# Kernel optimization log

Measured on AMD Instinct MI355X. Metric: run time of the kernel, lower is better.

The kernel has to match this reference:

```python
import jax, jax.numpy as jnp
import numpy as np

B, N, P, E, H, D, F, L = 16, 500, 100, 128, 8, 16, 512, 6
CLIP = 10.0  # logit_clipping


def _heads(x, h):
    b, n, _ = x.shape
    return x.reshape(b, n, h, -1).transpose(0, 2, 1, 3)  # [b,h,n,d]


def _mha(q, k, v, mask3=None):
    d = q.shape[-1]
    s = jnp.einsum('bhnd,bhmd->bhnm', q, k) / jnp.sqrt(jnp.asarray(d, q.dtype))
    if mask3 is not None:
        s = s + mask3[:, None, :, :]
    w = jax.nn.softmax(s, axis=-1)
    o = jnp.einsum('bhnm,bhmd->bhnd', w, v)
    b, h, n, dd = o.shape
    return o.transpose(0, 2, 1, 3).reshape(b, n, h * dd)


def _ff(x, w1, b1, w2, b2):
    return jax.nn.relu(x @ w1 + b1) @ w2 + b2


def _forward(depot_xy, node_xy, node_demand, load, cur_dist, ninf_mask,
             emb_depot_w, emb_depot_b, emb_node_w, emb_node_b,
             enc_wq, enc_wk, enc_wv, enc_comb_w, enc_comb_b,
             enc_ff1_w, enc_ff1_b, enc_ff2_w, enc_ff2_b,
             dec_wq_last, dec_wk, dec_wv, dec_comb_w, dec_comb_b,
             dec_cap_w, dec_ff1_w, dec_ff1_b, dec_ff2_w, dec_ff2_b,
             current_node):
    # ---------------- encoder ----------------
    node_xy_demand = jnp.concatenate([node_xy, node_demand[:, :, None]], axis=2)  # [B,N,3]
    x = jnp.concatenate([depot_xy @ emb_depot_w + emb_depot_b,
                         node_xy_demand @ emb_node_w + emb_node_b], axis=1)  # [B,N+1,E]
    for i in range(L):
        q = _heads(x @ enc_wq[i], H)
        k = _heads(x @ enc_wk[i], H)
        v = _heads(x @ enc_wv[i], H)
        mh = _mha(q, k, v) @ enc_comb_w[i] + enc_comb_b[i]
        o1 = x + mh
        x = o1 + _ff(o1, enc_ff1_w[i], enc_ff1_b[i], enc_ff2_w[i], enc_ff2_b[i])
    encoded_nodes = x  # [B, N+1, E]
    # decoder kv cache (set_kv)
    k = _heads(encoded_nodes @ dec_wk, H)
    v = _heads(encoded_nodes @ dec_wv, H)
    # ---------------- one decode step ----------------
    encoded_last = jnp.take_along_axis(encoded_nodes, current_node[:, :, None], axis=1)  # [B,P,E]
    input_cat = jnp.concatenate([encoded_last, load[:, :, None]], axis=2)  # [B,P,E+1]
    q = _heads(input_cat @ dec_wq_last, H)
    mh = _mha(q, k, v, mask3=ninf_mask) @ dec_comb_w + dec_comb_b
    mh = mh + encoded_last + load[:, :, None] @ dec_cap_w
    q_ref = _ff(mh, dec_ff1_w, dec_ff1_b, dec_ff2_w, dec_ff2_b) + mh
    score = jnp.einsum('bpe,bne->bpn', q_ref, encoded_nodes) / jnp.sqrt(jnp.asarray(E, q_ref.dtype))
    # distance-based noise injection
    dmin = cur_dist.min(axis=-1, keepdims=True)
    dmax = cur_dist.max(axis=-1, keepdims=True)
    norm_dist = (cur_dist - dmin) / (dmax - dmin + 1e-6)
    problem_size = ninf_mask.shape[2]
    nm = 50.0 / problem_size
    base_noise = jax.random.normal(jax.random.key(42), cur_dist.shape, cur_dist.dtype) * 0.2 + 0.5
    score = score - (1.0 - nm) * jnp.log(norm_dist + 1e-6) + base_noise * nm
    score = CLIP * jnp.tanh(score) + ninf_mask
    return jax.nn.softmax(score, axis=2)  # [B,P,N+1]


def setup_inputs() -> dict:
    key = jax.random.key(0)
    ks = iter(jax.random.split(key, 40))
    def rn(shape, s=0.02):
        return s * jax.random.normal(next(ks), shape, jnp.float32)
    return dict(
        depot_xy=jax.random.uniform(next(ks), (B, 1, 2), jnp.float32),
        node_xy=jax.random.uniform(next(ks), (B, N, 2), jnp.float32),
        node_demand=jax.random.uniform(next(ks), (B, N), jnp.float32),
        load=jax.random.uniform(next(ks), (B, P), jnp.float32),
        cur_dist=jax.random.uniform(next(ks), (B, P, N + 1), jnp.float32),
        ninf_mask=jnp.zeros((B, P, N + 1), jnp.float32),
        current_node=jax.random.randint(next(ks), (B, P), 0, N + 1),
        emb_depot_w=rn((2, E)), emb_depot_b=rn((E,)),
        emb_node_w=rn((3, E)), emb_node_b=rn((E,)),
        enc_wq=rn((L, E, H * D)), enc_wk=rn((L, E, H * D)), enc_wv=rn((L, E, H * D)),
        enc_comb_w=rn((L, H * D, E)), enc_comb_b=rn((L, E)),
        enc_ff1_w=rn((L, E, F)), enc_ff1_b=rn((L, F)),
        enc_ff2_w=rn((L, F, E)), enc_ff2_b=rn((L, E)),
        dec_wq_last=rn((E + 1, H * D)), dec_wk=rn((E, H * D)), dec_wv=rn((E, H * D)),
        dec_comb_w=rn((H * D, E)), dec_comb_b=rn((E,)),
        dec_cap_w=rn((1, E)),
        dec_ff1_w=rn((E, F)), dec_ff1_b=rn((F,)),
        dec_ff2_w=rn((F, E)), dec_ff2_b=rn((E,)),
    )


def reference(depot_xy, node_xy, node_demand, load, cur_dist, ninf_mask, current_node,
              emb_depot_w, emb_depot_b, emb_node_w, emb_node_b,
              enc_wq, enc_wk, enc_wv, enc_comb_w, enc_comb_b,
              enc_ff1_w, enc_ff1_b, enc_ff2_w, enc_ff2_b,
              dec_wq_last, dec_wk, dec_wv, dec_comb_w, dec_comb_b,
              dec_cap_w, dec_ff1_w, dec_ff1_b, dec_ff2_w, dec_ff2_b):
    return _forward(depot_xy, node_xy, node_demand, load, cur_dist, ninf_mask,
                    emb_depot_w, emb_depot_b, emb_node_w, emb_node_b,
                    enc_wq, enc_wk, enc_wv, enc_comb_w, enc_comb_b,
                    enc_ff1_w, enc_ff1_b, enc_ff2_w, enc_ff2_b,
                    dec_wq_last, dec_wk, dec_wv, dec_comb_w, dec_comb_b,
                    dec_cap_w, dec_ff1_w, dec_ff1_b, dec_ff2_w, dec_ff2_b,
                    current_node)
```

## Files before the change

kernel.cpp:

```cpp
#include <hip/hip_runtime.h>
#include <math.h>

#define Bb 16
#define Nn 500
#define NT 501
#define Pp 100
#define Ee 128
#define Hh 8
#define Dd 16
#define Ff 512
#define Ll 6
#define Mtok (Bb*NT)
#define PR (Bb*Pp)
#define TJ 32
#define SPLIT 4
#define KSEG 126
#define DSPLIT 16
#define DSEG 32
#define ENCP (6*128*384)
#define DECP (128*256)
#define SNP 512
#define KP 36

typedef __attribute__((ext_vector_type(8))) short bf16x8;
typedef __attribute__((ext_vector_type(4))) float f32x4;

__device__ __forceinline__ unsigned short bfhi(float x){
  union { float f; unsigned u; } c; c.f = x; return (unsigned short)(c.u >> 16);
}
__device__ __forceinline__ float bff(unsigned short h){
  union { float f; unsigned u; } c; c.u = ((unsigned)h) << 16; return c.f;
}
__device__ __forceinline__ uint2 pack4(unsigned short a, unsigned short b,
                                       unsigned short c, unsigned short d){
  uint2 r; r.x = (unsigned)a | ((unsigned)b << 16);
  r.y = (unsigned)c | ((unsigned)d << 16); return r;
}

__global__ __launch_bounds__(256) void pack_k(
    const float* __restrict__ ewq, const float* __restrict__ ewk, const float* __restrict__ ewv,
    const float* __restrict__ dwk, const float* __restrict__ dwv,
    float* __restrict__ encP, float* __restrict__ decP)
{
  int i = blockIdx.x*256 + threadIdx.x;
  if (i < ENCP) {
    int l = i / (128*384); int rem = i - l*128*384; int k = rem / 384; int n = rem - k*384;
    float v;
    if (n < 128)      v = ewq[((size_t)l*128 + k)*128 + n];
    else if (n < 256) v = ewk[((size_t)l*128 + k)*128 + (n-128)];
    else              v = ewv[((size_t)l*128 + k)*128 + (n-256)];
    encP[i] = v;
  } else {
    int j = i - ENCP;
    if (j < DECP) {
      int k = j >> 8; int n = j & 255;
      decP[j] = (n < 128) ? dwk[k*128 + n] : dwv[k*128 + (n-128)];
    }
  }
}

__global__ __launch_bounds__(256) void embed_k(
    const float* __restrict__ depot_xy, const float* __restrict__ node_xy,
    const float* __restrict__ node_demand,
    const float* __restrict__ wD, const float* __restrict__ bD,
    const float* __restrict__ wN, const float* __restrict__ bN,
    float* __restrict__ x)
{
  int t = blockIdx.x*256 + threadIdx.x;
  if (t >= Mtok*Ee) return;
  int e   = t & (Ee-1);
  int tok = t >> 7;
  int b   = tok / NT;
  int n   = tok - b*NT;
  float v;
  if (n == 0) {
    v = depot_xy[b*2+0]*wD[0*Ee+e] + depot_xy[b*2+1]*wD[1*Ee+e] + bD[e];
  } else {
    int nn = n - 1;
    float c0 = node_xy[(b*Nn + nn)*2 + 0];
    float c1 = node_xy[(b*Nn + nn)*2 + 1];
    float c2 = node_demand[b*Nn + nn];
    v = c0*wN[0*Ee+e] + c1*wN[1*Ee+e] + c2*wN[2*Ee+e] + bN[e];
  }
  x[(size_t)tok*Ee + e] = v;
}

__global__ __launch_bounds__(256) void gemm_k(
    const float* __restrict__ A, const float* __restrict__ W,
    const float* __restrict__ bias, const float* __restrict__ res,
    float* __restrict__ C, int M, int N, int K, int relu)
{
  __shared__ __align__(16) unsigned short Ah[2][64][KP];
  __shared__ __align__(16) unsigned short Al[2][64][KP];
  __shared__ __align__(16) unsigned short Bh[2][64][KP];
  __shared__ __align__(16) unsigned short Bl[2][64][KP];

  int tid = threadIdx.x;
  int m0 = blockIdx.x * 64, n0 = blockIdx.y * 64;
  int wvid = tid >> 6;
  int lane = tid & 63;
  int lrow = lane & 15;
  int lk8  = (lane >> 4) * 8;

  f32x4 acc0 = {0.f,0.f,0.f,0.f}, acc1 = acc0, acc2 = acc0, acc3 = acc0;

  int ar = tid >> 2;
  int ac = (tid & 3) << 2;
  int wr = tid >> 4;
  int wc = (tid & 15) << 2;

  const float* Ap = A + (size_t)(m0 + ar)*K + ac;
  const float* Wp = W + (size_t)wr*N + n0 + wc;
  bool aok = (m0 + ar) < M;

  float4 zz = make_float4(0.f,0.f,0.f,0.f);
  float4 av0 = aok ? *(const float4*)(Ap)      : zz;
  float4 av1 = aok ? *(const float4*)(Ap + 16) : zz;
  float4 wv0 = *(const float4*)(Wp);
  float4 wv1 = *(const float4*)(Wp + (size_t)16*N);

  int nk = K >> 5;
  for (int t = 0; t < nk; ++t) {
    int cur = t & 1;
    {
      unsigned short h0=bfhi(av0.x), h1=bfhi(av0.y), h2=bfhi(av0.z), h3=bfhi(av0.w);
      unsigned short l0=bfhi(av0.x-bff(h0)), l1=bfhi(av0.y-bff(h1)),
                     l2=bfhi(av0.z-bff(h2)), l3=bfhi(av0.w-bff(h3));
      *(uint2*)&Ah[cur][ar][ac] = pack4(h0,h1,h2,h3);
      *(uint2*)&Al[cur][ar][ac] = pack4(l0,l1,l2,l3);
      h0=bfhi(av1.x); h1=bfhi(av1.y); h2=bfhi(av1.z); h3=bfhi(av1.w);
      l0=bfhi(av1.x-bff(h0)); l1=bfhi(av1.y-bff(h1));
      l2=bfhi(av1.z-bff(h2)); l3=bfhi(av1.w-bff(h3));
      *(uint2*)&Ah[cur][ar][ac+16] = pack4(h0,h1,h2,h3);
      *(uint2*)&Al[cur][ar][ac+16] = pack4(l0,l1,l2,l3);
    }
    {
      float w4[4] = {wv0.x, wv0.y, wv0.z, wv0.w};
      #pragma unroll
      for (int i=0;i<4;i++){
        unsigned short h = bfhi(w4[i]);
        Bh[cur][wc+i][wr] = h;
        Bl[cur][wc+i][wr] = bfhi(w4[i] - bff(h));
      }
      float w5[4] = {wv1.x, wv1.y, wv1.z, wv1.w};
      #pragma unroll
      for (int i=0;i<4;i++){
        unsigned short h = bfhi(w5[i]);
        Bh[cur][wc+i][wr+16] = h;
        Bl[cur][wc+i][wr+16] = bfhi(w5[i] - bff(h));
      }
    }
    __syncthreads();
    if (t+1 < nk) {
      av0 = aok ? *(const float4*)(Ap + (size_t)(t+1)*32)      : zz;
      av1 = aok ? *(const float4*)(Ap + (size_t)(t+1)*32 + 16) : zz;
      wv0 = *(const float4*)(Wp + (size_t)(t+1)*32*N);
      wv1 = *(const float4*)(Wp + ((size_t)(t+1)*32 + 16)*N);
    }
    union FR { bf16x8 v; uint2 u[2]; };
    FR ah, al;
    ah.u[0] = *(const uint2*)&Ah[cur][wvid*16 + lrow][lk8];
    ah.u[1] = *(const uint2*)&Ah[cur][wvid*16 + lrow][lk8+4];
    al.u[0] = *(const uint2*)&Al[cur][wvid*16 + lrow][lk8];
    al.u[1] = *(const uint2*)&Al[cur][wvid*16 + lrow][lk8+4];
    #define DOFRAG(f, accv) { \
      FR bh, bl; \
      bh.u[0] = *(const uint2*)&Bh[cur][(f)*16 + lrow][lk8]; \
      bh.u[1] = *(const uint2*)&Bh[cur][(f)*16 + lrow][lk8+4]; \
      bl.u[0] = *(const uint2*)&Bl[cur][(f)*16 + lrow][lk8]; \
      bl.u[1] = *(const uint2*)&Bl[cur][(f)*16 + lrow][lk8+4]; \
      accv = __builtin_amdgcn_mfma_f32_16x16x32_bf16(ah.v, bh.v, accv, 0,0,0); \
      accv = __builtin_amdgcn_mfma_f32_16x16x32_bf16(ah.v, bl.v, accv, 0,0,0); \
      accv = __builtin_amdgcn_mfma_f32_16x16x32_bf16(al.v, bh.v, accv, 0,0,0); \
    }
    DOFRAG(0, acc0); DOFRAG(1, acc1); DOFRAG(2, acc2); DOFRAG(3, acc3);
    #undef DOFRAG
  }

  int crow0 = m0 + wvid*16 + (lane >> 4)*4;
  int col0  = n0 + lrow;
  #define WRFRAG(f, accv) { \
    int col = col0 + (f)*16; \
    float bvs = bias ? bias[col] : 0.f; \
    _Pragma("unroll") \
    for (int j=0;j<4;j++){ \
      int row = crow0 + j; \
      if (row < M) { \
        float v = accv[j] + bvs; \
        if (relu) v = fmaxf(v, 0.f); \
        if (res) v += res[(size_t)row*N + col]; \
        C[(size_t)row*N + col] = v; \
      } \
    } \
  }
  WRFRAG(0, acc0); WRFRAG(1, acc1); WRFRAG(2, acc2); WRFRAG(3, acc3);
  #undef WRFRAG
}

__device__ __forceinline__ float dot4(float4 a, float4 b){
  return fmaf(a.x,b.x, fmaf(a.y,b.y, fmaf(a.z,b.z, a.w*b.w)));
}

__global__ __launch_bounds__(256, 1) void attn_enc_k(
    const float* __restrict__ QKV, float* __restrict__ part_o,
    float* __restrict__ part_l)
{
  int blk = blockIdx.x;
  int s  = blk % SPLIT;
  int bh = blk / SPLIT;
  int h  = bh & (Hh-1);
  int b  = bh >> 3;
  int tid = threadIdx.x;
  int p0 = tid;
  int p1 = tid + 256;
  const int klo = s*KSEG;
  int kseg = NT - klo; if (kseg > KSEG) kseg = KSEG;

  __shared__ __align__(16) float4 Ks[2][TJ][4];
  __shared__ __align__(16) float4 Vs[2][TJ][4];

  int row = (tid >> 2) & 31;
  int lc  = tid & 3;
  bool isV = tid >= 128;
  const int kvoff = isV ? 256 : 128;

  bool vbq = p1 < NT;

  const float4* qp0 = (const float4*)(QKV + ((size_t)(b*NT + p0))*384 + h*Dd);
  float4 qa0=qp0[0], qa1=qp0[1], qa2=qp0[2], qa3=qp0[3];
  float4 qb0,qb1,qb2,qb3;
  if (vbq) {
    const float4* qp1 = (const float4*)(QKV + ((size_t)(b*NT + p1))*384 + h*Dd);
    qb0=qp1[0]; qb1=qp1[1]; qb2=qp1[2]; qb3=qp1[3];
  } else {
    qb0=qb1=qb2=qb3=make_float4(0,0,0,0);
  }

  if (row < kseg) {
    float4 v = *((const float4*)(QKV + ((size_t)(b*NT + klo + row))*384 + kvoff + h*Dd) + lc);
    if (isV) Vs[0][row][lc] = v; else Ks[0][row][lc] = v;
  }
  __syncthreads();

  float lA = 0.f, lB = 0.f;
  float4 oA0=make_float4(0,0,0,0), oA1=oA0, oA2=oA0, oA3=oA0;
  float4 oB0=oA0, oB1=oA0, oB2=oA0, oB3=oA0;
  const int ntiles = (kseg + TJ - 1)/TJ;
  int buf = 0;

  for (int t = 0; t < ntiles; ++t) {
    int j0 = t*TJ;
    if (t+1 < ntiles) {
      int jj = j0 + TJ + row;
      if (jj < kseg) {
        float4 v = *((const float4*)(QKV + ((size_t)(b*NT + klo + jj))*384 + kvoff + h*Dd) + lc);
        if (isV) Vs[buf^1][row][lc] = v; else Ks[buf^1][row][lc] = v;
      }
    }
    int jend = kseg - j0; if (jend > TJ) jend = TJ;

    #pragma unroll 2
    for (int jj = 0; jj < jend; ++jj) {
      float4 k0=Ks[buf][jj][0], k1=Ks[buf][jj][1], k2=Ks[buf][jj][2], k3=Ks[buf][jj][3];
      float sA = (dot4(qa0,k0)+dot4(qa1,k1)) + (dot4(qa2,k2)+dot4(qa3,k3));
      float sB = (dot4(qb0,k0)+dot4(qb1,k1)) + (dot4(qb2,k2)+dot4(qb3,k3));
      float wA = __expf(sA*0.25f);
      float wB = __expf(sB*0.25f);
      lA += wA; lB += wB;
      float4 v0=Vs[buf][jj][0], v1=Vs[buf][jj][1], v2=Vs[buf][jj][2], v3=Vs[buf][jj][3];
      oA0.x=fmaf(wA,v0.x,oA0.x); oA0.y=fmaf(wA,v0.y,oA0.y); oA0.z=fmaf(wA,v0.z,oA0.z); oA0.w=fmaf(wA,v0.w,oA0.w);
      oA1.x=fmaf(wA,v1.x,oA1.x); oA1.y=fmaf(wA,v1.y,oA1.y); oA1.z=fmaf(wA,v1.z,oA1.z); oA1.w=fmaf(wA,v1.w,oA1.w);
      oA2.x=fmaf(wA,v2.x,oA2.x); oA2.y=fmaf(wA,v2.y,oA2.y); oA2.z=fmaf(wA,v2.z,oA2.z); oA2.w=fmaf(wA,v2.w,oA2.w);
      oA3.x=fmaf(wA,v3.x,oA3.x); oA3.y=fmaf(wA,v3.y,oA3.y); oA3.z=fmaf(wA,v3.z,oA3.z); oA3.w=fmaf(wA,v3.w,oA3.w);
      oB0.x=fmaf(wB,v0.x,oB0.x); oB0.y=fmaf(wB,v0.y,oB0.y); oB0.z=fmaf(wB,v0.z,oB0.z); oB0.w=fmaf(wB,v0.w,oB0.w);
      oB1.x=fmaf(wB,v1.x,oB1.x); oB1.y=fmaf(wB,v1.y,oB1.y); oB1.z=fmaf(wB,v1.z,oB1.z); oB1.w=fmaf(wB,v1.w,oB1.w);
      oB2.x=fmaf(wB,v2.x,oB2.x); oB2.y=fmaf(wB,v2.y,oB2.y); oB2.z=fmaf(wB,v2.z,oB2.z); oB2.w=fmaf(wB,v2.w,oB2.w);
      oB3.x=fmaf(wB,v3.x,oB3.x); oB3.y=fmaf(wB,v3.y,oB3.y); oB3.z=fmaf(wB,v3.z,oB3.z); oB3.w=fmaf(wB,v3.w,oB3.w);
    }
    __syncthreads();
    buf ^= 1;
  }

  size_t r0 = ((size_t)s*128 + bh)*NT + p0;
  float4* po0 = (float4*)(part_o + r0*16);
  po0[0]=oA0; po0[1]=oA1; po0[2]=oA2; po0[3]=oA3;
  part_l[r0] = lA;
  if (vbq) {
    size_t r1 = ((size_t)s*128 + bh)*NT + p1;
    float4* po1 = (float4*)(part_o + r1*16);
    po1[0]=oB0; po1[1]=oB1; po1[2]=oB2; po1[3]=oB3;
    part_l[r1] = lB;
  }
}

__global__ __launch_bounds__(256) void comb_gemm_k(
    const float* __restrict__ part_o, const float* __restrict__ part_l,
    const float* __restrict__ W, const float* __restrict__ bias,
    const float* __restrict__ res, float* __restrict__ C)
{
  __shared__ __align__(16) float As[2][16][68];
  __shared__ __align__(16) float Bs[2][16][68];
  int tid = threadIdx.x;
  int tx = tid & 15, ty = tid >> 4;
  int m0 = blockIdx.x * 64, n0 = blockIdx.y * 64;
  float acc[4][4];
  #pragma unroll
  for (int i=0;i<4;i++)
    #pragma unroll
    for (int j=0;j<4;j++) acc[i][j] = 0.f;

  int ar = tid >> 2;
  int ak = (tid & 3) << 2;
  int br = tid >> 4;
  int bc = (tid & 15) << 2;

  int row = m0 + ar;
  bool aok = row < Mtok;
  int tok = aok ? row : 0;
  int bb = tok / NT;
  int p  = tok - bb*NT;
  const size_t pbase = ((size_t)(bb*8))*NT + p;

  const float* Wp = W + (size_t)br*Ee + n0 + bc;

  #define LOADA(t, dst) { \
    float4 o4 = make_float4(0.f,0.f,0.f,0.f); float l = 0.f; \
    _Pragma("unroll") \
    for (int s=0;s<SPLIT;s++){ \
      size_t idx = (size_t)s*((size_t)128*NT) + pbase + (size_t)(t)*NT; \
      float4 v = *(const float4*)(part_o + idx*16 + ak); \
      o4.x+=v.x; o4.y+=v.y; o4.z+=v.z; o4.w+=v.w; \
      l += part_l[idx]; \
    } \
    float inv = aok ? 1.f/l : 0.f; \
    dst = make_float4(o4.x*inv, o4.y*inv, o4.z*inv, o4.w*inv); \
  }

  float4 av; LOADA(0, av);
  float4 wv = *(const float4*)(Wp);

  for (int t = 0; t < 8; ++t) {
    int cur = t & 1;
    As[cur][ak+0][ar] = av.x; As[cur][ak+1][ar] = av.y;
    As[cur][ak+2][ar] = av.z; As[cur][ak+3][ar] = av.w;
    *(float4*)(&Bs[cur][br][bc]) = wv;
    __syncthreads();
    if (t+1 < 8) {
      LOADA(t+1, av);
      wv = *(const float4*)(Wp + (size_t)(t+1)*16*Ee);
    }
    #pragma unroll
    for (int k=0;k<16;k++){
      float4 a4 = *(const float4*)(&As[cur][k][ty*4]);
      float4 b4 = *(const float4*)(&Bs[cur][k][tx*4]);
      float avv[4] = {a4.x,a4.y,a4.z,a4.w};
      float bvv[4] = {b4.x,b4.y,b4.z,b4.w};
      #pragma unroll
      for (int i=0;i<4;i++)
        #pragma unroll
        for (int j=0;j<4;j++)
          acc[i][j] = fmaf(avv[i], bvv[j], acc[i][j]);
    }
  }
  #undef LOADA

  float4 bv = *(const float4*)(bias + n0 + tx*4);
  #pragma unroll
  for (int i=0;i<4;i++){
    int orow = m0 + ty*4 + i;
    if (orow >= Mtok) continue;
    float4 o;
    float4 rv = *(const float4*)(res + (size_t)orow*Ee + n0 + tx*4);
    o.x = acc[i][0] + bv.x + rv.x; o.y = acc[i][1] + bv.y + rv.y;
    o.z = acc[i][2] + bv.z + rv.z; o.w = acc[i][3] + bv.w + rv.w;
    *(float4*)(C + (size_t)orow*Ee + n0 + tx*4) = o;
  }
}

__global__ __launch_bounds__(128) void attn_dec_k(
    const float* __restrict__ Q, const float* __restrict__ KV,
    const float* __restrict__ mask,
    float* __restrict__ part_o, float* __restrict__ part_l)
{
  int blk = blockIdx.x;
  int s  = blk & (DSPLIT-1);
  int bh = blk >> 4;
  int h  = bh & (Hh-1);
  int b  = bh >> 3;
  int klo = s*DSEG;
  int kn  = NT - klo; if (kn > DSEG) kn = DSEG;

  __shared__ __align__(16) float4 Ks[DSEG][4];
  __shared__ __align__(16) float4 Vs[DSEG][4];

  int tid = threadIdx.x;
  for (int i = tid; i < kn*8; i += 128) {
    int row  = i >> 3;
    int q8   = i & 7;
    int quad = q8 & 3;
    int isv  = q8 >> 2;
    float4 v = *(const float4*)(KV + ((size_t)(b*NT + klo + row))*256 + isv*128 + h*Dd + quad*4);
    if (isv) Vs[row][quad] = v; else Ks[row][quad] = v;
  }
  __syncthreads();

  int p = tid;
  if (p >= Pp) return;
  int r = b*Pp + p;
  const float4* qp = (const float4*)(Q + (size_t)r*Ee + h*Dd);
  float4 qa=qp[0], qb=qp[1], qc=qp[2], qd=qp[3];
  const float* mrow = mask + (size_t)r*NT + klo;

  float l = 0.f;
  float4 o0=make_float4(0,0,0,0), o1=o0, o2=o0, o3=o0;
  for (int j=0;j<kn;++j){
    float sc = (dot4(qa,Ks[j][0])+dot4(qb,Ks[j][1])) + (dot4(qc,Ks[j][2])+dot4(qd,Ks[j][3]));
    float w = __expf(sc*0.25f + mrow[j]);
    l += w;
    float4 v0=Vs[j][0],v1=Vs[j][1],v2=Vs[j][2],v3=Vs[j][3];
    o0.x=fmaf(w,v0.x,o0.x); o0.y=fmaf(w,v0.y,o0.y); o0.z=fmaf(w,v0.z,o0.z); o0.w=fmaf(w,v0.w,o0.w);
    o1.x=fmaf(w,v1.x,o1.x); o1.y=fmaf(w,v1.y,o1.y); o1.z=fmaf(w,v1.z,o1.z); o1.w=fmaf(w,v1.w,o1.w);
    o2.x=fmaf(w,v2.x,o2.x); o2.y=fmaf(w,v2.y,o2.y); o2.z=fmaf(w,v2.z,o2.z); o2.w=fmaf(w,v2.w,o2.w);
    o3.x=fmaf(w,v3.x,o3.x); o3.y=fmaf(w,v3.y,o3.y); o3.z=fmaf(w,v3.z,o3.z); o3.w=fmaf(w,v3.w,o3.w);
  }

  size_t rb = ((size_t)s*PR + r)*Hh + h;
  float4* po = (float4*)(part_o + rb*16);
  po[0]=o0; po[1]=o1; po[2]=o2; po[3]=o3;
  part_l[rb] = l;
}

__global__ __launch_bounds__(128) void decq_k(
    const float* __restrict__ x, const int* __restrict__ cur,
    const float* __restrict__ loadv, const float* __restrict__ Wq,
    float* __restrict__ q, float* __restrict__ encl)
{
  __shared__ float row[Ee];
  int r = blockIdx.x, e = threadIdx.x;
  int b = r / Pp;
  int node = cur[r];
  float xv = x[((size_t)(b*NT + node))*Ee + e];
  encl[(size_t)r*Ee + e] = xv;
  row[e] = xv;
  __syncthreads();
  float acc = 0.f;
  #pragma unroll 4
  for (int k=0;k<Ee;k++) acc = fmaf(row[k], Wq[k*128 + e], acc);
  acc = fmaf(loadv[r], Wq[Ee*128 + e], acc);
  q[(size_t)r*128 + e] = acc;
}

__global__ __launch_bounds__(128) void dec_comb_k(
    const float* __restrict__ dpart_o, const float* __restrict__ dpart_l,
    const float* __restrict__ W, const float* __restrict__ bias,
    const float* __restrict__ encl, const float* __restrict__ loadv,
    const float* __restrict__ capw, float* __restrict__ mh)
{
  __shared__ float row[Ee];
  int r = blockIdx.x, e = threadIdx.x;
  int h = e >> 4, d = e & 15;
  const size_t S = (size_t)PR*Hh;
  size_t rb = (size_t)r*Hh + h;
  float L = 0.f, o = 0.f;
  #pragma unroll
  for (int s=0;s<DSPLIT;s++){
    L += dpart_l[(size_t)s*S + rb];
    o += dpart_o[((size_t)s*S + rb)*16 + d];
  }
  row[e] = o / L;
  __syncthreads();
  float acc = 0.f;
  #pragma unroll 4
  for (int k=0;k<Ee;k++) acc = fmaf(row[k], W[k*Ee + e], acc);
  mh[(size_t)r*Ee + e] = acc + bias[e] + encl[(size_t)r*Ee + e] + loadv[r]*capw[e];
}

__global__ __launch_bounds__(256) void xt_k(
    const float* __restrict__ x, float* __restrict__ xT)
{
  __shared__ float T[32][33];
  int n0 = blockIdx.x * 32;
  int k0 = blockIdx.y * 32;
  int b  = blockIdx.z;
  int t  = threadIdx.x;
  int row = t >> 3;
  int c4  = (t & 7) << 2;

  int n = n0 + row;
  float4 v = make_float4(0.f,0.f,0.f,0.f);
  if (n < NT) v = *(const float4*)(x + ((size_t)(b*NT + n))*Ee + k0 + c4);
  T[c4+0][row] = v.x; T[c4+1][row] = v.y; T[c4+2][row] = v.z; T[c4+3][row] = v.w;
  __syncthreads();

  const float SC = 0.08838834764831845f;
  float4 o;
  o.x = T[row][c4+0]*SC; o.y = T[row][c4+1]*SC;
  o.z = T[row][c4+2]*SC; o.w = T[row][c4+3]*SC;
  *(float4*)(xT + ((size_t)(b*Ee + k0 + row))*SNP + n0 + c4) = o;
}

__global__ __launch_bounds__(256) void score_gemm_k(
    const float* __restrict__ qref, const float* __restrict__ xT,
    float* __restrict__ score)
{
  __shared__ __align__(16) float As[2][16][68];
  __shared__ __align__(16) float Bs[2][16][68];
  int tid = threadIdx.x;
  int tx = tid & 15, ty = tid >> 4;
  int m0 = blockIdx.x * 64;
  int n0 = blockIdx.y * 64;
  int b  = blockIdx.z;

  const float* A = qref + (size_t)b*Pp*Ee;
  const float* W = xT   + (size_t)b*Ee*SNP;
  float*       C = score + (size_t)b*Pp*SNP;

  float acc[4][4];
  #pragma unroll
  for (int i=0;i<4;i++)
    #pragma unroll
    for (int j=0;j<4;j++) acc[i][j] = 0.f;

  int ar = tid >> 2;
  int ak = (tid & 3) << 2;
  int br = tid >> 4;
  int bc = (tid & 15) << 2;

  const float* Ap = A + (size_t)(m0 + ar)*Ee + ak;
  const float* Wp = W + (size_t)br*SNP + n0 + bc;
  bool aok = (m0 + ar) < Pp;

  float4 av = aok ? *(const float4*)(Ap) : make_float4(0.f,0.f,0.f,0.f);
  float4 wv = *(const float4*)(Wp);

  for (int t = 0; t < 8; ++t) {
    int cur = t & 1;
    As[cur][ak+0][ar] = av.x; As[cur][ak+1][ar] = av.y;
    As[cur][ak+2][ar] = av.z; As[cur][ak+3][ar] = av.w;
    *(float4*)(&Bs[cur][br][bc]) = wv;
    __syncthreads();
    if (t+1 < 8) {
      av = aok ? *(const float4*)(Ap + (t+1)*16) : make_float4(0.f,0.f,0.f,0.f);
      wv = *(const float4*)(Wp + (size_t)(t+1)*16*SNP);
    }
    #pragma unroll
    for (int k=0;k<16;k++){
      float4 a4 = *(const float4*)(&As[cur][k][ty*4]);
      float4 b4 = *(const float4*)(&Bs[cur][k][tx*4]);
      float avv[4] = {a4.x,a4.y,a4.z,a4.w};
      float bvv[4] = {b4.x,b4.y,b4.z,b4.w};
      #pragma unroll
      for (int i=0;i<4;i++)
        #pragma unroll
        for (int j=0;j<4;j++)
          acc[i][j] = fmaf(avv[i], bvv[j], acc[i][j]);
    }
    __syncthreads();
  }

  #pragma unroll
  for (int i=0;i<4;i++){
    int row = m0 + ty*4 + i;
    if (row >= Pp) continue;
    float4 o;
    o.x = acc[i][0]; o.y = acc[i][1]; o.z = acc[i][2]; o.w = acc[i][3];
    *(float4*)(C + (size_t)row*SNP + n0 + tx*4) = o;
  }
}

__device__ __forceinline__ unsigned rotl32(unsigned x, int r){ return (x<<r)|(x>>(32-r)); }

__device__ float tf_normal(unsigned idx)
{
  unsigned x0 = 0u;
  unsigned x1 = idx;
  const unsigned ks[3] = {0u, 42u, 0u ^ 42u ^ 0x1BD11BDAu};
  x0 += ks[0]; x1 += ks[1];
  const int rotA[4] = {13,15,26,6};
  const int rotB[4] = {17,29,16,24};
  #pragma unroll
  for (int i=0;i<5;i++){
    #pragma unroll
    for (int q=0;q<4;q++){
      int rr = (i&1) ? rotB[q] : rotA[q];
      x0 += x1; x1 = rotl32(x1, rr); x1 ^= x0;
    }
    x0 += ks[(i+1)%3];
    x1 += ks[(i+2)%3] + (unsigned)(i+1);
  }
  unsigned bits = x0 ^ x1;
  float f = __uint_as_float((bits >> 9) | 0x3f800000u) - 1.0f;
  const float lo = -0.99999994f;
  float u = f * 2.0f + lo;
  u = fmaxf(lo, u);
  float w = -log1pf(-u*u);
  float p;
  if (w < 5.0f) {
    w -= 2.5f;
    p = 2.81022636e-08f;
    p = fmaf(p, w, 3.43273939e-07f);
    p = fmaf(p, w, -3.5233877e-06f);
    p = fmaf(p, w, -4.39150654e-06f);
    p = fmaf(p, w, 0.00021858087f);
    p = fmaf(p, w, -0.00125372503f);
    p = fmaf(p, w, -0.00417768164f);
    p = fmaf(p, w, 0.246640727f);
    p = fmaf(p, w, 1.50140941f);
  } else {
    w = sqrtf(w) - 3.0f;
    p = -0.000200214257f;
    p = fmaf(p, w, 0.000100950558f);
    p = fmaf(p, w, 0.00134934322f);
    p = fmaf(p, w, -0.00367342844f);
    p = fmaf(p, w, 0.00573950773f);
    p = fmaf(p, w, -0.0076224613f);
    p = fmaf(p, w, 0.00943887047f);
    p = fmaf(p, w, 1.00167406f);
    p = fmaf(p, w, 2.83297682f);
  }
  return 1.4142135623730951f * (p * u);
}

__global__ __launch_bounds__(512) void final_k(
    const float* __restrict__ score, const float* __restrict__ cur_dist,
    const float* __restrict__ ninf, float* __restrict__ out)
{
  __shared__ float smn[8], smx[8], sm2[8], ss[8];
  const float NM = (float)(50.0/501.0);
  const float C1 = (float)(1.0 - 50.0/501.0);
  int r = blockIdx.x;
  int t = threadIdx.x;
  int wid = t >> 6, lane = t & 63;

  float cd = 0.f;
  float mn = 1e30f, mx = -1e30f;
  if (t < NT) { cd = cur_dist[(size_t)r*NT + t]; mn = cd; mx = cd; }
  #pragma unroll
  for (int off=32; off>=1; off>>=1){
    mn = fminf(mn, __shfl_xor(mn, off));
    mx = fmaxf(mx, __shfl_xor(mx, off));
  }
  if (lane == 0){ smn[wid] = mn; smx[wid] = mx; }
  __syncthreads();
  float dmin = smn[0], dmax = smx[0];
  #pragma unroll
  for (int i=1;i<8;i++){ dmin = fminf(dmin, smn[i]); dmax = fmaxf(dmax, smx[i]); }

  float sval = -1e30f;
  if (t < NT) {
    float nd = (cd - dmin) / (dmax - dmin + 1e-6f);
    float z  = tf_normal((unsigned)r*501u + (unsigned)t);
    float s  = score[(size_t)r*SNP + t] - C1*logf(nd + 1e-6f) + (z*0.2f + 0.5f)*NM;
    sval = 10.0f*tanhf(s) + ninf[(size_t)r*NT + t];
  }
  float mv = sval;
  #pragma unroll
  for (int off=32; off>=1; off>>=1) mv = fmaxf(mv, __shfl_xor(mv, off));
  if (lane == 0) sm2[wid] = mv;
  __syncthreads();
  float smax = sm2[0];
  #pragma unroll
  for (int i=1;i<8;i++) smax = fmaxf(smax, sm2[i]);

  float e = (t < NT) ? expf(sval - smax) : 0.f;
  float sv = e;
  #pragma unroll
  for (int off=32; off>=1; off>>=1) sv += __shfl_xor(sv, off);
  if (lane == 0) ss[wid] = sv;
  __syncthreads();
  float ssum = ss[0];
  #pragma unroll
  for (int i=1;i<8;i++) ssum += ss[i];

  if (t < NT) out[(size_t)r*NT + t] = e / ssum;
}

extern "C" void kernel_launch(void* const* d_in, const int* in_sizes, int n_in,
                              void* d_out, int out_size, void* d_ws, size_t ws_size,
                              hipStream_t stream)
{
  (void)in_sizes; (void)n_in; (void)out_size; (void)ws_size;
  const float* depot_xy    = (const float*)d_in[0];
  const float* node_xy     = (const float*)d_in[1];
  const float* node_demand = (const float*)d_in[2];
  const float* loadv       = (const float*)d_in[3];
  const float* cur_dist    = (const float*)d_in[4];
  const float* ninf        = (const float*)d_in[5];
  const int*   cur_node    = (const int*)d_in[6];
  const float* emb_depot_w = (const float*)d_in[7];
  const float* emb_depot_b = (const float*)d_in[8];
  const float* emb_node_w  = (const float*)d_in[9];
  const float* emb_node_b  = (const float*)d_in[10];
  const float* enc_wq      = (const float*)d_in[11];
  const float* enc_wk      = (const float*)d_in[12];
  const float* enc_wv      = (const float*)d_in[13];
  const float* enc_comb_w  = (const float*)d_in[14];
  const float* enc_comb_b  = (const float*)d_in[15];
  const float* enc_ff1_w   = (const float*)d_in[16];
  const float* enc_ff1_b   = (const float*)d_in[17];
  const float* enc_ff2_w   = (const float*)d_in[18];
  const float* enc_ff2_b   = (const float*)d_in[19];
  const float* dec_wq_last = (const float*)d_in[20];
  const float* dec_wk      = (const float*)d_in[21];
  const float* dec_wv      = (const float*)d_in[22];
  const float* dec_comb_w  = (const float*)d_in[23];
  const float* dec_comb_b  = (const float*)d_in[24];
  const float* dec_cap_w   = (const float*)d_in[25];
  const float* dec_ff1_w   = (const float*)d_in[26];
  const float* dec_ff1_b   = (const float*)d_in[27];
  const float* dec_ff2_w   = (const float*)d_in[28];
  const float* dec_ff2_b   = (const float*)d_in[29];

  float* ws = (float*)d_ws;
  const size_t SZ = (size_t)Mtok*Ee;
  float* xb    = ws + 0*SZ;
  float* qkvb  = ws + 1*SZ;
  float* atb   = ws + 4*SZ;
  float* o1b   = ws + 5*SZ;
  float* ffb   = ws + 6*SZ;
  float* encPk = ws + 10*SZ;
  float* decPk = encPk + ENCP;
  float* part_o  = ffb;
  float* epart_l = atb;
  float* dpart_o = ffb;
  float* dpart_l = o1b;
  float* encl  = qkvb + 2*SZ;
  float* qdec  = encl + 204800;
  float* mhb   = qdec + 204800;
  float* qrefb = atb;
  float* ffh2  = ffb;
  float* xTb   = ffb;
  float* scoreb= o1b;

  pack_k<<<(ENCP + DECP + 255)/256, 256, 0, stream>>>(
      enc_wq, enc_wk, enc_wv, dec_wk, dec_wv, encPk, decPk);

  embed_k<<<(Mtok*Ee + 255)/256, 256, 0, stream>>>(
      depot_xy, node_xy, node_demand, emb_depot_w, emb_depot_b,
      emb_node_w, emb_node_b, xb);

  dim3 gqkv((Mtok + 63)/64, 384/64);
  dim3 gcombg((Mtok + 63)/64, Ee/64);
  dim3 gff ((Mtok + 63)/64, Ff/64);
  dim3 g128((Mtok + 63)/64, Ee/64);
  for (int l = 0; l < Ll; ++l) {
    gemm_k<<<gqkv, 256, 0, stream>>>(xb, encPk + (size_t)l*128*384, nullptr, nullptr, qkvb, Mtok, 384, Ee, 0);
    attn_enc_k<<<Bb*Hh*SPLIT, 256, 0, stream>>>(qkvb, part_o, epart_l);
    comb_gemm_k<<<gcombg, 256, 0, stream>>>(part_o, epart_l, enc_comb_w + (size_t)l*Ee*Ee,
                                            enc_comb_b + l*Ee, xb, o1b);
    gemm_k<<<gff, 256, 0, stream>>>(o1b, enc_ff1_w + (size_t)l*Ee*Ff, enc_ff1_b + l*Ff, nullptr, ffb, Mtok, Ff, Ee, 1);
    gemm_k<<<g128, 256, 0, stream>>>(ffb, enc_ff2_w + (size_t)l*Ff*Ee, enc_ff2_b + l*Ee, o1b, xb, Mtok, Ee, Ff, 0);
  }

  dim3 gkv((Mtok + 63)/64, 256/64);
  gemm_k<<<gkv, 256, 0, stream>>>(xb, decPk, nullptr, nullptr, qkvb, Mtok, 256, Ee, 0);
  decq_k<<<PR, 128, 0, stream>>>(xb, cur_node, loadv, dec_wq_last, qdec, encl);
  attn_dec_k<<<Bb*Hh*DSPLIT, 128, 0, stream>>>(qdec, qkvb, ninf, dpart_o, dpart_l);
  dec_comb_k<<<PR, 128, 0, stream>>>(dpart_o, dpart_l, dec_comb_w, dec_comb_b, encl, loadv, dec_cap_w, mhb);
  dim3 gd1((PR + 63)/64, Ff/64);
  gemm_k<<<gd1, 256, 0, stream>>>(mhb, dec_ff1_w, dec_ff1_b, nullptr, ffh2, PR, Ff, Ee, 1);
  dim3 gd2((PR + 63)/64, Ee/64);
  gemm_k<<<gd2, 256, 0, stream>>>(ffh2, dec_ff2_w, dec_ff2_b, mhb, qrefb, PR, Ee, Ff, 0);
  dim3 gxt(16, 4, 16);
  xt_k<<<gxt, 256, 0, stream>>>(xb, xTb);
  dim3 gsc(2, 8, 16);
  score_gemm_k<<<gsc, 256, 0, stream>>>(qrefb, xTb, scoreb);
  final_k<<<PR, 512, 0, stream>>>(scoreb, cur_dist, ninf, (float*)d_out);
}
```

Baseline: 980.5 us.

## Pre-transpose and pre-split GEMM weights into packed bf16 hi/lo words

Adds a pre-pass kernel that transposes each weight matrix to N-major layout and packs every element into a 32-bit word holding its bf16 high and low parts. The GEMM then loads contiguous uint4 weight chunks and uses byte-permute instructions to write vectorized LDS stores. This replaces the per-tile float-to-bf16 split and the scattered transposed 16-bit LDS stores. In exchange it adds six small packing launches per call and extra workspace memory.

```diff
diff --git a/kernel.cpp b/kernel.cpp
--- a/kernel.cpp
+++ b/kernel.cpp
@@ -36,6 +36,11 @@
   uint2 r; r.x = (unsigned)a | ((unsigned)b << 16);
   r.y = (unsigned)c | ((unsigned)d << 16); return r;
 }
+__device__ __forceinline__ unsigned pkhl(float f){
+  unsigned short h = bfhi(f);
+  unsigned short l = bfhi(f - bff(h));
+  return (unsigned)h | ((unsigned)l << 16);
+}
 
 __global__ __launch_bounds__(256) void pack_k(
     const float* __restrict__ ewq, const float* __restrict__ ewk, const float* __restrict__ ewv,
@@ -57,6 +62,27 @@
       decP[j] = (n < 128) ? dwk[k*128 + n] : dwv[k*128 + (n-128)];
     }
   }
+}
+
+__global__ __launch_bounds__(256) void wt_pack_k(
+    const float* __restrict__ src, unsigned* __restrict__ dst, int K, int N)
+{
+  src += (size_t)blockIdx.z * K * N;
+  dst += (size_t)blockIdx.z * K * N;
+  __shared__ float T[32][33];
+  int n0 = blockIdx.x * 32, k0 = blockIdx.y * 32;
+  int t = threadIdx.x;
+  int row = t >> 3;
+  int c4  = (t & 7) << 2;
+
+  float4 v = *(const float4*)(src + (size_t)(k0 + row)*N + n0 + c4);
+  T[c4+0][row] = v.x; T[c4+1][row] = v.y; T[c4+2][row] = v.z; T[c4+3][row] = v.w;
+  __syncthreads();
+
+  uint4 o;
+  o.x = pkhl(T[row][c4+0]); o.y = pkhl(T[row][c4+1]);
+  o.z = pkhl(T[row][c4+2]); o.w = pkhl(T[row][c4+3]);
+  *(uint4*)(dst + (size_t)(n0 + row)*K + k0 + c4) = o;
 }
 
 __global__ __launch_bounds__(256) void embed_k(
@@ -86,7 +112,7 @@
 }
 
 __global__ __launch_bounds__(256) void gemm_k(
-    const float* __restrict__ A, const float* __restrict__ W,
+    const float* __restrict__ A, const unsigned* __restrict__ Wt,
     const float* __restrict__ bias, const float* __restrict__ res,
     float* __restrict__ C, int M, int N, int K, int relu)
 {
@@ -106,18 +132,18 @@
 
   int ar = tid >> 2;
   int ac = (tid & 3) << 2;
-  int wr = tid >> 4;
-  int wc = (tid & 15) << 2;
-
   const float* Ap = A + (size_t)(m0 + ar)*K + ac;
-  const float* Wp = W + (size_t)wr*N + n0 + wc;
   bool aok = (m0 + ar) < M;
+
+  int wr2 = tid >> 2;
+  int wcu = (tid & 3) << 3;
+  const unsigned* Wp = Wt + (size_t)(n0 + wr2)*K + wcu;
 
   float4 zz = make_float4(0.f,0.f,0.f,0.f);
   float4 av0 = aok ? *(const float4*)(Ap)      : zz;
   float4 av1 = aok ? *(const float4*)(Ap + 16) : zz;
-  float4 wv0 = *(const float4*)(Wp);
-  float4 wv1 = *(const float4*)(Wp + (size_t)16*N);
+  uint4 w0 = *(const uint4*)(Wp);
+  uint4 w1 = *(const uint4*)(Wp + 4);
 
   int nk = K >> 5;
   for (int t = 0; t < nk; ++t) {
@@ -135,27 +161,25 @@
       *(uint2*)&Al[cur][ar][ac+16] = pack4(l0,l1,l2,l3);
     }
     {
-      float w4[4] = {wv0.x, wv0.y, wv0.z, wv0.w};
-      #pragma unroll
-      for (int i=0;i<4;i++){
-        unsigned short h = bfhi(w4[i]);
-        Bh[cur][wc+i][wr] = h;
-        Bl[cur][wc+i][wr] = bfhi(w4[i] - bff(h));
-      }
-      float w5[4] = {wv1.x, wv1.y, wv1.z, wv1.w};
-      #pragma unroll
-      for (int i=0;i<4;i++){
-        unsigned short h = bfhi(w5[i]);
-        Bh[cur][wc+i][wr+16] = h;
-        Bl[cur][wc+i][wr+16] = bfhi(w5[i] - bff(h));
-      }
+      unsigned bh0=__builtin_amdgcn_perm(w0.y,w0.x,0x05040100u);
+      unsigned bh1=__builtin_amdgcn_perm(w0.w,w0.z,0x05040100u);
+      unsigned bh2=__builtin_amdgcn_perm(w1.y,w1.x,0x05040100u);
+      unsigned bh3=__builtin_amdgcn_perm(w1.w,w1.z,0x05040100u);
+      unsigned bl0=__builtin_amdgcn_perm(w0.y,w0.x,0x07060302u);
+      unsigned bl1=__builtin_amdgcn_perm(w0.w,w0.z,0x07060302u);
+      unsigned bl2=__builtin_amdgcn_perm(w1.y,w1.x,0x07060302u);
+      unsigned bl3=__builtin_amdgcn_perm(w1.w,w1.z,0x07060302u);
+      *(uint2*)&Bh[cur][wr2][wcu]   = make_uint2(bh0,bh1);
+      *(uint2*)&Bh[cur][wr2][wcu+4] = make_uint2(bh2,bh3);
+      *(uint2*)&Bl[cur][wr2][wcu]   = make_uint2(bl0,bl1);
+      *(uint2*)&Bl[cur][wr2][wcu+4] = make_uint2(bl2,bl3);
     }
     __syncthreads();
     if (t+1 < nk) {
       av0 = aok ? *(const float4*)(Ap + (size_t)(t+1)*32)      : zz;
       av1 = aok ? *(const float4*)(Ap + (size_t)(t+1)*32 + 16) : zz;
-      wv0 = *(const float4*)(Wp + (size_t)(t+1)*32*N);
-      wv1 = *(const float4*)(Wp + ((size_t)(t+1)*32 + 16)*N);
+      w0 = *(const uint4*)(Wp + (size_t)(t+1)*32);
+      w1 = *(const uint4*)(Wp + (size_t)(t+1)*32 + 4);
     }
     union FR { bf16x8 v; uint2 u[2]; };
     FR ah, al;
@@ -720,6 +744,12 @@
   float* ffb   = ws + 6*SZ;
   float* encPk = ws + 10*SZ;
   float* decPk = encPk + ENCP;
+  unsigned* qkvT = (unsigned*)(decPk + DECP);
+  unsigned* ff1T = qkvT + (size_t)6*384*128;
+  unsigned* ff2T = ff1T + (size_t)6*512*128;
+  unsigned* dkvT = ff2T + (size_t)6*128*512;
+  unsigned* d1T  = dkvT + 256*128;
+  unsigned* d2T  = d1T + 512*128;
   float* part_o  = ffb;
   float* epart_l = atb;
   float* dpart_o = ffb;
@@ -734,6 +764,12 @@
 
   pack_k<<<(ENCP + DECP + 255)/256, 256, 0, stream>>>(
       enc_wq, enc_wk, enc_wv, dec_wk, dec_wv, encPk, decPk);
+  wt_pack_k<<<dim3(384/32, 128/32, 6), 256, 0, stream>>>(encPk, qkvT, 128, 384);
+  wt_pack_k<<<dim3(512/32, 128/32, 6), 256, 0, stream>>>(enc_ff1_w, ff1T, 128, 512);
+  wt_pack_k<<<dim3(128/32, 512/32, 6), 256, 0, stream>>>(enc_ff2_w, ff2T, 512, 128);
+  wt_pack_k<<<dim3(256/32, 128/32, 1), 256, 0, stream>>>(decPk, dkvT, 128, 256);
+  wt_pack_k<<<dim3(512/32, 128/32, 1), 256, 0, stream>>>(dec_ff1_w, d1T, 128, 512);
+  wt_pack_k<<<dim3(128/32, 512/32, 1), 256, 0, stream>>>(dec_ff2_w, d2T, 512, 128);
 
   embed_k<<<(Mtok*Ee + 255)/256, 256, 0, stream>>>(
       depot_xy, node_xy, node_demand, emb_depot_w, emb_depot_b,
@@ -744,23 +780,23 @@
   dim3 gff ((Mtok + 63)/64, Ff/64);
   dim3 g128((Mtok + 63)/64, Ee/64);
   for (int l = 0; l < Ll; ++l) {
-    gemm_k<<<gqkv, 256, 0, stream>>>(xb, encPk + (size_t)l*128*384, nullptr, nullptr, qkvb, Mtok, 384, Ee, 0);
+    gemm_k<<<gqkv, 256, 0, stream>>>(xb, qkvT + (size_t)l*384*128, nullptr, nullptr, qkvb, Mtok, 384, Ee, 0);
     attn_enc_k<<<Bb*Hh*SPLIT, 256, 0, stream>>>(qkvb, part_o, epart_l);
     comb_gemm_k<<<gcombg, 256, 0, stream>>>(part_o, epart_l, enc_comb_w + (size_t)l*Ee*Ee,
                                             enc_comb_b + l*Ee, xb, o1b);
-    gemm_k<<<gff, 256, 0, stream>>>(o1b, enc_ff1_w + (size_t)l*Ee*Ff, enc_ff1_b + l*Ff, nullptr, ffb, Mtok, Ff, Ee, 1);
-    gemm_k<<<g128, 256, 0, stream>>>(ffb, enc_ff2_w + (size_t)l*Ff*Ee, enc_ff2_b + l*Ee, o1b, xb, Mtok, Ee, Ff, 0);
+    gemm_k<<<gff, 256, 0, stream>>>(o1b, ff1T + (size_t)l*512*128, enc_ff1_b + l*Ff, nullptr, ffb, Mtok, Ff, Ee, 1);
+    gemm_k<<<g128, 256, 0, stream>>>(ffb, ff2T + (size_t)l*128*512, enc_ff2_b + l*Ee, o1b, xb, Mtok, Ee, Ff, 0);
   }
 
   dim3 gkv((Mtok + 63)/64, 256/64);
-  gemm_k<<<gkv, 256, 0, stream>>>(xb, decPk, nullptr, nullptr, qkvb, Mtok, 256, Ee, 0);
+  gemm_k<<<gkv, 256, 0, stream>>>(xb, dkvT, nullptr, nullptr, qkvb, Mtok, 256, Ee, 0);
   decq_k<<<PR, 128, 0, stream>>>(xb, cur_node, loadv, dec_wq_last, qdec, encl);
   attn_dec_k<<<Bb*Hh*DSPLIT, 128, 0, stream>>>(qdec, qkvb, ninf, dpart_o, dpart_l);
   dec_comb_k<<<PR, 128, 0, stream>>>(dpart_o, dpart_l, dec_comb_w, dec_comb_b, encl, loadv, dec_cap_w, mhb);
   dim3 gd1((PR + 63)/64, Ff/64);
-  gemm_k<<<gd1, 256, 0, stream>>>(mhb, dec_ff1_w, dec_ff1_b, nullptr, ffh2, PR, Ff, Ee, 1);
+  gemm_k<<<gd1, 256, 0, stream>>>(mhb, d1T, dec_ff1_b, nullptr, ffh2, PR, Ff, Ee, 1);
   dim3 gd2((PR + 63)/64, Ee/64);
-  gemm_k<<<gd2, 256, 0, stream>>>(ffh2, dec_ff2_w, dec_ff2_b, mhb, qrefb, PR, Ee, Ff, 0);
+  gemm_k<<<gd2, 256, 0, stream>>>(ffh2, d2T, dec_ff2_b, mhb, qrefb, PR, Ee, Ff, 0);
   dim3 gxt(16, 4, 16);
   xt_k<<<gxt, 256, 0, stream>>>(xb, xTb);
   dim3 gsc(2, 8, 16);
```

Result: no change. 974.6 us (-0.6%).
